# Performance work log

Measured on AMD Instinct MI355X. Metric: run time of the kernel, lower is better.

Reference implementation:

```python
import jax, jax.numpy as jnp
import numpy as np

# dims
L, E, D, DFF, H = 4, 4, 512, 2048, 8
B, T, S, K = 16, 256, 512, 2
HD = D // H


def _ln(x, g, b, eps=1e-5):
    m = x.mean(-1, keepdims=True)
    v = ((x - m) ** 2).mean(-1, keepdims=True)
    return (x - m) / jnp.sqrt(v + eps) * g + b


def _mha(xq, xkv, in_w, in_b, out_w, out_b):
    # torch nn.MultiheadAttention (batch_first), no masks, eval mode
    qw, kw, vw = jnp.split(in_w, 3, axis=0)
    qb, kb, vb = jnp.split(in_b, 3)
    q = xq @ qw.T + qb                       # [B,T,D]
    k = xkv @ kw.T + kb                      # [B,S,D]
    v = xkv @ vw.T + vb
    def heads(t):
        b, s, _ = t.shape
        return t.reshape(b, s, H, HD).transpose(0, 2, 1, 3)
    q, k, v = heads(q), heads(k), heads(v)   # [B,H,*,HD]
    scale = 1.0 / float(np.sqrt(HD))
    a = jax.nn.softmax(jnp.einsum('bhtd,bhsd->bhts', q, k) * scale, axis=-1)
    o = jnp.einsum('bhts,bhsd->bhtd', a, v)
    o = o.transpose(0, 2, 1, 3).reshape(xq.shape[0], xq.shape[1], D)
    return o @ out_w.T + out_b


def _expert(p, x, mem):
    (siw, sib, sow, sob, ciw, cib, cow, cob,
     l1w, l1b, l2w, l2b, g1, b1, g2, b2, g3, b3) = p
    sa = _mha(x, x, siw, sib, sow, sob)
    x = _ln(x + sa, g1, b1)
    ca = _mha(x, mem, ciw, cib, cow, cob)
    x = _ln(x + ca, g2, b2)
    ffn = jax.nn.relu(x @ l1w.T + l1b) @ l2w.T + l2b
    x = _ln(x + ffn, g3, b3)
    return x


def _forward(tgt, memory, router_w, params):
    x = tgt
    for l in range(L):
        pooled = x.mean(axis=1)                      # [B,D] sample-level routing
        logits = pooled @ router_w[l].T              # [B,E]
        vals, idx = jax.lax.top_k(logits, K)
        w = jax.nn.softmax(vals.astype(jnp.float32), axis=-1).astype(x.dtype)
        # dense [B,E] combine weights: zero for unselected experts -> same math
        wf = jnp.zeros((x.shape[0], E), x.dtype).at[jnp.arange(x.shape[0])[:, None], idx].add(w)
        p_l = jax.tree_util.tree_map(lambda a: a[l], params)   # each [E,...]
        outs = jax.vmap(_expert, in_axes=(0, None, None))(p_l, x, memory)  # [E,B,T,D]
        x = jnp.einsum('be,ebtd->btd', wf, outs)
    return x


def setup_inputs() -> dict:
    key = jax.random.key(0)
    ks = jax.random.split(key, 16)
    n = lambda k, shape: jax.random.normal(k, shape, jnp.float32) * 0.02
    return {
        'tgt': jax.random.normal(ks[0], (B, T, D), jnp.float32),
        'memory': jax.random.normal(ks[1], (B, S, D), jnp.float32),
        'router_w': n(ks[2], (L, E, D)),
        'sa_in_w': n(ks[3], (L, E, 3 * D, D)), 'sa_in_b': jnp.zeros((L, E, 3 * D)),
        'sa_out_w': n(ks[4], (L, E, D, D)), 'sa_out_b': jnp.zeros((L, E, D)),
        'ca_in_w': n(ks[5], (L, E, 3 * D, D)), 'ca_in_b': jnp.zeros((L, E, 3 * D)),
        'ca_out_w': n(ks[6], (L, E, D, D)), 'ca_out_b': jnp.zeros((L, E, D)),
        'lin1_w': n(ks[7], (L, E, DFF, D)), 'lin1_b': jnp.zeros((L, E, DFF)),
        'lin2_w': n(ks[8], (L, E, D, DFF)), 'lin2_b': jnp.zeros((L, E, D)),
        'n1_g': jnp.ones((L, E, D)), 'n1_b': jnp.zeros((L, E, D)),
        'n2_g': jnp.ones((L, E, D)), 'n2_b': jnp.zeros((L, E, D)),
        'n3_g': jnp.ones((L, E, D)), 'n3_b': jnp.zeros((L, E, D)),
    }


def reference(tgt, memory, router_w, sa_in_w, sa_in_b, sa_out_w, sa_out_b,
              ca_in_w, ca_in_b, ca_out_w, ca_out_b, lin1_w, lin1_b, lin2_w, lin2_b,
              n1_g, n1_b, n2_g, n2_b, n3_g, n3_b):
    params = (sa_in_w, sa_in_b, sa_out_w, sa_out_b, ca_in_w, ca_in_b, ca_out_w, ca_out_b,
              lin1_w, lin1_b, lin2_w, lin2_b, n1_g, n1_b, n2_g, n2_b, n3_g, n3_b)
    return _forward(tgt, memory, router_w, params)
```

## Files before the change

kernel.cpp:

```cpp
#include <hip/hip_runtime.h>
#include <hip/hip_bf16.h>

#define L_ 4
#define E_ 4
#define D_ 512
#define DFF_ 2048
#define H_ 8
#define B_ 16
#define T_ 256
#define S_ 512
#define HD_ 64
#define NSLOT 32

typedef __attribute__((ext_vector_type(4))) float f32x4;
typedef __attribute__((ext_vector_type(8))) short bf16x8;
typedef __attribute__((ext_vector_type(4))) int i32x4;

static __device__ __forceinline__ float bf2f(unsigned short u){
  union{float f; unsigned u;} c; c.u = ((unsigned)u)<<16; return c.f;
}
static __device__ __forceinline__ unsigned short f2bf(float f){
  union{float f; unsigned u;} c; c.f=f;
  unsigned u=c.u;
  return (unsigned short)((u + 0x7FFFu + ((u>>16)&1u))>>16);
}

static __device__ __forceinline__ void gload16(const unsigned short* g, unsigned short* l){
  __builtin_amdgcn_global_load_lds(
      (const __attribute__((address_space(1))) void*)g,
      (__attribute__((address_space(3))) void*)l, 16, 0, 0);
}

static __device__ __forceinline__ int xcd_swz(int orig, int nwg){
  int q = nwg >> 3, r = nwg & 7;
  int xcd = orig & 7, idx = orig >> 3;
  return (xcd < r) ? (xcd*(q+1) + idx) : (r*(q+1) + (xcd-r)*q + idx);
}

__global__ void __launch_bounds__(256) pool_k(const float* __restrict__ x,
    float* __restrict__ part)
{
  int b = blockIdx.x >> 3, ch = blockIdx.x & 7;
  int tid = threadIdx.x;
  const float* xp = x + ((long)b*T_ + ch*32)*D_ + tid*2;
  float s0=0.f, s1=0.f;
  #pragma unroll 8
  for (int t=0;t<32;t++){
    float2 v = *(const float2*)(xp + (long)t*D_);
    s0 += v.x; s1 += v.y;
  }
  float* pp = part + ((long)b*8 + ch)*D_ + tid*2;
  pp[0]=s0; pp[1]=s1;
}

__global__ void __launch_bounds__(256) route2_k(const float* __restrict__ part,
    const float* __restrict__ rw, int* __restrict__ eidx, float* __restrict__ wgt)
{
  __shared__ float pooled[D_];
  __shared__ float logit[E_];
  int b = blockIdx.x, tid = threadIdx.x;
  for (int d = tid; d < D_; d += 256){
    float s = 0.f;
    #pragma unroll
    for (int c=0;c<8;c++) s += part[((long)b*8 + c)*D_ + d];
    pooled[d] = s * (1.f/T_);
  }
  __syncthreads();
  int wave = tid>>6, lane = tid&63;
  {
    float s=0.f;
    const float* w = rw + (long)wave*D_;
    for (int d=lane; d<D_; d+=64) s += pooled[d]*w[d];
    #pragma unroll
    for (int o=32;o;o>>=1) s += __shfl_xor(s,o);
    if (lane==0) logit[wave] = s;
  }
  __syncthreads();
  if (tid==0){
    int i1=0; float v1=logit[0];
    for (int e=1;e<E_;e++) if (logit[e] > v1){ v1=logit[e]; i1=e; }
    int i2=-1; float v2=-3.4e38f;
    for (int e=0;e<E_;e++) if (e!=i1 && logit[e] > v2){ v2=logit[e]; i2=e; }
    float e2 = __expf(v2 - v1);
    float w1 = 1.f/(1.f+e2);
    eidx[2*b]=i1; eidx[2*b+1]=i2;
    wgt[2*b]=w1; wgt[2*b+1]=e2*w1;
  }
}

__global__ void __launch_bounds__(256) cast_bf16_k(const float* __restrict__ in,
    unsigned short* __restrict__ out, long n){
  long i = ((long)blockIdx.x*blockDim.x + threadIdx.x)*4;
  long st = (long)gridDim.x*blockDim.x*4;
  for (; i<n; i+=st){
    float4 v = *(const float4*)(in+i);
    ushort4 o; o.x=f2bf(v.x); o.y=f2bf(v.y); o.z=f2bf(v.z); o.w=f2bf(v.w);
    *(ushort4*)(out+i) = o;
  }
}

__global__ void __launch_bounds__(256) cast_weights_k(
    const float* __restrict__ s0, const float* __restrict__ s1,
    const float* __restrict__ s2, const float* __restrict__ s3,
    const float* __restrict__ s4, const float* __restrict__ s5,
    unsigned short* __restrict__ d0, unsigned short* __restrict__ d1,
    unsigned short* __restrict__ d2, unsigned short* __restrict__ d3,
    unsigned short* __restrict__ d4, unsigned short* __restrict__ d5)
{
  const long N0=(long)E_*3*D_*D_, N1=(long)E_*D_*D_;
  const long N2=N0, N3=N1, N4=(long)E_*DFF_*D_, N5=N4;
  const long total = N0+N1+N2+N3+N4+N5;
  long i = ((long)blockIdx.x*256 + threadIdx.x)*4;
  long st = (long)gridDim.x*256*4;
  for (; i<total; i+=st){
    const float* s; unsigned short* d; long j = i;
    if (j < N0){ s=s0; d=d0; }
    else if ((j-=N0) < N1){ s=s1; d=d1; }
    else if ((j-=N1) < N2){ s=s2; d=d2; }
    else if ((j-=N2) < N3){ s=s3; d=d3; }
    else if ((j-=N3) < N4){ s=s4; d=d4; }
    else { j-=N4; s=s5; d=d5; }
    float4 v = *(const float4*)(s+j);
    ushort4 o; o.x=f2bf(v.x); o.y=f2bf(v.y); o.z=f2bf(v.z); o.w=f2bf(v.w);
    *(ushort4*)(d+j) = o;
  }
}

__global__ void __launch_bounds__(256) vtrans2_k(
    const unsigned short* __restrict__ src0, long sSlot0, int ld0,
    unsigned short* __restrict__ dst0, int rows0,
    const unsigned short* __restrict__ src1, long sSlot1, int ld1,
    unsigned short* __restrict__ dst1, int rows1)
{
  __shared__ unsigned short t[64][68];
  int xb = blockIdx.x;
  const unsigned short* src; long sSlot; int ld; unsigned short* dst; int rows; int s0;
  if (xb < rows0/64){ src=src0; sSlot=sSlot0; ld=ld0; dst=dst0; rows=rows0; s0=xb*64; }
  else              { src=src1; sSlot=sSlot1; ld=ld1; dst=dst1; rows=rows1; s0=(xb-rows0/64)*64; }
  int h = blockIdx.y; int slot = blockIdx.z;
  const unsigned short* sp = src + (long)slot*sSlot + (long)h*64;
  int c = threadIdx.x&63, w = threadIdx.x>>6;
  #pragma unroll
  for (int i=0;i<16;i++){
    int r = i*4 + w;
    t[r][c] = sp[(long)(s0+r)*ld + c];
  }
  __syncthreads();
  unsigned short* dp = dst + ((long)slot*H_ + h)*((long)64*rows) + s0;
  #pragma unroll
  for (int i=0;i<16;i++){
    int d = i*4 + w;
    dp[(long)d*rows + c] = t[c][d];
  }
}

template<int NT>
__global__ void __launch_bounds__(512) fattn_k(
    const unsigned short* __restrict__ Qg, long qSlot, int ldq,
    const unsigned short* __restrict__ Kg, long kSlot, int ldk,
    const unsigned short* __restrict__ Vtg,
    unsigned short* __restrict__ Og, long oSlot, int ldo)
{
  constexpr int SLEN = NT*64;
  constexpr int NT2 = NT/2;
  __shared__ unsigned short K_lds[128][72];
  __shared__ unsigned short V_lds[64][136];
  __shared__ unsigned short P_lds[8][16][72];

  int nwg = gridDim.x*gridDim.y;
  int wg = xcd_swz(blockIdx.x + gridDim.x*blockIdx.y, nwg);
  int qb = wg % gridDim.x;
  int z  = wg / gridDim.x;
  int slot = z >> 3, h = z & 7;
  int tid = threadIdx.x, wave = tid>>6, lane = tid&63;
  int lr = lane&15, lg = lane>>4;
  int lk = lg*8;

  const unsigned short* Qp = Qg + (long)slot*qSlot + (long)h*HD_;
  const unsigned short* Kp = Kg + (long)slot*kSlot + (long)h*HD_;
  const unsigned short* Vp = Vtg + (long)z*((long)HD_*SLEN);

  bf16x8 qf[2];
  {
    int qrow = qb*128 + wave*16 + lr;
    const unsigned short* qr = Qp + (long)qrow*ldq;
    qf[0] = *(const bf16x8*)(qr + lk);
    qf[1] = *(const bf16x8*)(qr + 32 + lk);
  }

  float m_prev[4], l_run[4];
  f32x4 acc_o[4];
  #pragma unroll
  for (int r=0;r<4;r++){ m_prev[r]=-1e30f; l_run[r]=0.f; }
  #pragma unroll
  for (int ni=0;ni<4;ni++) acc_o[ni]=(f32x4){0.f,0.f,0.f,0.f};

  int srow = tid>>3, sch = tid&7;

  i32x4 kr0 = *(const i32x4*)(Kp + (long)srow*ldk + sch*8);
  i32x4 kr1 = *(const i32x4*)(Kp + (long)(srow+64)*ldk + sch*8);
  i32x4 vr0 = *(const i32x4*)(Vp + (long)srow*SLEN + sch*8);
  i32x4 vr1 = *(const i32x4*)(Vp + (long)srow*SLEN + 64 + sch*8);

  for (int it=0; it<NT2; ++it){
    __syncthreads();
    *(i32x4*)&K_lds[srow][sch*8] = kr0;
    *(i32x4*)&K_lds[srow+64][sch*8] = kr1;
    *(i32x4*)&V_lds[srow][sch*8] = vr0;
    *(i32x4*)&V_lds[srow][64 + sch*8] = vr1;
    __syncthreads();

    int itn = (it+1 < NT2) ? it+1 : it;
    int k0n = itn*128;
    kr0 = *(const i32x4*)(Kp + (long)(k0n+srow)*ldk + sch*8);
    kr1 = *(const i32x4*)(Kp + (long)(k0n+srow+64)*ldk + sch*8);
    vr0 = *(const i32x4*)(Vp + (long)srow*SLEN + k0n + sch*8);
    vr1 = *(const i32x4*)(Vp + (long)srow*SLEN + k0n + 64 + sch*8);

    #pragma unroll
    for (int sub=0; sub<2; ++sub){
      f32x4 s[4];
      #pragma unroll
      for (int ni=0;ni<4;ni++) s[ni]=(f32x4){0.f,0.f,0.f,0.f};
      __builtin_amdgcn_s_setprio(1);
      #pragma unroll
      for (int ki=0;ki<2;ki++){
        #pragma unroll
        for (int ni=0;ni<4;ni++){
          bf16x8 kf = *(const bf16x8*)&K_lds[sub*64 + ni*16+lr][ki*32+lk];
          s[ni] = __builtin_amdgcn_mfma_f32_16x16x32_bf16(qf[ki], kf, s[ni],0,0,0);
        }
      }
      __builtin_amdgcn_s_setprio(0);
      float tmax[4];
      #pragma unroll
      for (int r=0;r<4;r++){
        tmax[r] = fmaxf(fmaxf(s[0][r],s[1][r]),fmaxf(s[2][r],s[3][r]));
        #pragma unroll
        for (int msk=1; msk<16; msk<<=1) tmax[r]=fmaxf(tmax[r], __shfl_xor(tmax[r],msk));
      }
      bool inc = (tmax[0]>m_prev[0])|(tmax[1]>m_prev[1])|(tmax[2]>m_prev[2])|(tmax[3]>m_prev[3]);
      if (__any(inc)){
        #pragma unroll
        for (int r=0;r<4;r++){
          float mnew = fmaxf(m_prev[r], tmax[r]);
          float corr = __expf(m_prev[r]-mnew);
          m_prev[r] = mnew;
          l_run[r] *= corr;
          #pragma unroll
          for (int ni=0;ni<4;ni++) acc_o[ni][r] *= corr;
        }
      }
      float rs[4] = {0.f,0.f,0.f,0.f};
      #pragma unroll
      for (int ni=0;ni<4;ni++){
        #pragma unroll
        for (int r=0;r<4;r++){
          float p = __expf(s[ni][r]-m_prev[r]);
          rs[r] += p;
          P_lds[wave][lg*4+r][ni*16+lr] = f2bf(p);
        }
      }
      #pragma unroll
      for (int r=0;r<4;r++){
        #pragma unroll
        for (int msk=1; msk<16; msk<<=1) rs[r] += __shfl_xor(rs[r],msk);
        l_run[r] += rs[r];
      }
      __builtin_amdgcn_s_setprio(1);
      #pragma unroll
      for (int ki=0;ki<2;ki++){
        bf16x8 pf = *(const bf16x8*)&P_lds[wave][lr][ki*32+lk];
        #pragma unroll
        for (int ni=0;ni<4;ni++){
          bf16x8 vf = *(const bf16x8*)&V_lds[ni*16+lr][sub*64 + ki*32+lk];
          acc_o[ni] = __builtin_amdgcn_mfma_f32_16x16x32_bf16(pf, vf, acc_o[ni],0,0,0);
        }
      }
      __builtin_amdgcn_s_setprio(0);
    }
  }
  unsigned short* Op = Og + (long)slot*oSlot + (long)h*HD_;
  #pragma unroll
  for (int r=0;r<4;r++){
    float inv = 1.f/l_run[r];
    int q = qb*128 + wave*16 + lg*4 + r;
    #pragma unroll
    for (int ni=0;ni<4;ni++)
      Op[(long)q*ldo + ni*16 + lr] = f2bf(acc_o[ni][r]*inv);
  }
}

template<int BM, int BN, int WTM, int WTN, int BK>
static __device__ __forceinline__ void gemm_core(
    const unsigned short* __restrict__ Ap,
    const unsigned short* __restrict__ Wp,
    const float* __restrict__ bp,
    void* __restrict__ Cp, long cbase, int ldc,
    int lda, int ldw, int bm0, int bn0,
    int K, int f32out, int relu, int scaleNlim, float scaleVal,
    unsigned short* smem)
{
  constexpr int WAVES_N = BN/WTN;
  constexpr int MI = WTM/16, NI = WTN/16;
  constexpr int SLOTS = BK/8;
  int tid  = threadIdx.x;
  int wave = tid>>6, lane = tid&63;
  int wm = wave / WAVES_N, wn = wave % WAVES_N;
  int lr = lane&15;
  int lg = lane>>4;
  int swz = (BK==64) ? (lr&7) : ((lr>>1)&3);

  f32x4 acc[MI][NI];
  #pragma unroll
  for (int i=0;i<MI;i++)
  #pragma unroll
  for (int j=0;j<NI;j++) acc[i][j] = (f32x4){0.f,0.f,0.f,0.f};

  auto stage = [&](int buf, int k0){
    unsigned short* as = &smem[(size_t)buf*(BM+BN)*BK];
    unsigned short* bs = as + BM*BK;
    #pragma unroll
    for (int i=0;i<BM*SLOTS/512;i++){
      int cch = i*512 + tid;
      int row = cch / SLOTS, c = cch % SLOTS;
      int cs = (BK==64) ? (c ^ (row&7)) : (c ^ ((row>>1)&3));
      gload16(Ap + (long)row*lda + k0 + (cs<<3), as + cch*8);
    }
    #pragma unroll
    for (int i=0;i<BN*SLOTS/512;i++){
      int cch = i*512 + tid;
      int row = cch / SLOTS, c = cch % SLOTS;
      int cs = (BK==64) ? (c ^ (row&7)) : (c ^ ((row>>1)&3));
      gload16(Wp + (long)row*ldw + k0 + (cs<<3), bs + cch*8);
    }
  };

  auto compute = [&](int buf){
    unsigned short* as = &smem[(size_t)buf*(BM+BN)*BK];
    unsigned short* bs = as + BM*BK;
    #pragma unroll
    for (int ki=0;ki<BK/32;ki++){
      bf16x8 af[MI], bfr[NI];
      #pragma unroll
      for (int mi=0;mi<MI;mi++){
        int row = wm*WTM + mi*16 + lr;
        af[mi] = *(const bf16x8*)&as[row*BK + (((ki*4+lg) ^ swz)<<3)];
      }
      #pragma unroll
      for (int ni=0;ni<NI;ni++){
        int row = wn*WTN + ni*16 + lr;
        bfr[ni] = *(const bf16x8*)&bs[row*BK + (((ki*4+lg) ^ swz)<<3)];
      }
      __builtin_amdgcn_s_setprio(1);
      #pragma unroll
      for (int mi=0;mi<MI;mi++)
      #pragma unroll
      for (int ni=0;ni<NI;ni++)
        acc[mi][ni] = __builtin_amdgcn_mfma_f32_16x16x32_bf16(af[mi], bfr[ni], acc[mi][ni], 0,0,0);
      __builtin_amdgcn_s_setprio(0);
    }
  };

  int NT = K / BK;
  stage(0, 0);
  __syncthreads();
  int cur = 0;
  for (int t=0; t<NT; ++t){
    if (t+1 < NT) stage(cur^1, (t+1)*BK);
    compute(cur);
    __syncthreads();
    cur ^= 1;
  }

  int rbase = lg*4;
  #pragma unroll
  for (int mi=0;mi<MI;mi++)
  #pragma unroll
  for (int ni=0;ni<NI;ni++){
    f32x4 v = acc[mi][ni];
    int n = bn0 + wn*WTN + ni*16 + lr;
    float bv = bp ? bp[n] : 0.f;
    float scv = (n < scaleNlim) ? scaleVal : 1.f;
    #pragma unroll
    for (int r=0;r<4;r++){
      int m = bm0 + wm*WTM + mi*16 + rbase + r;
      float val = (v[r] + bv) * scv;
      if (relu) val = fmaxf(val, 0.f);
      long o = cbase + (long)m*ldc + n;
      if (f32out) ((float*)Cp)[o] = val;
      else ((unsigned short*)Cp)[o] = f2bf(val);
    }
  }
}

template<int BM, int BN, int WTM, int WTN, int BK>
__global__ void __launch_bounds__(512) gemm_lds(
    const unsigned short* __restrict__ A, long aSlot, int aDiv, long aHead, int lda,
    const unsigned short* __restrict__ W, long wSlot, long wHead, long wExp, int ldw,
    const int* __restrict__ eidx, const float* __restrict__ bias, long biasExp,
    void* __restrict__ Cp, long cSlot, long cHead, int ldc,
    int K, int HZ, int f32out, int relu, int scaleNlim, float scaleVal)
{
  constexpr int SLOTS = BK/8;
  static_assert((BM/WTM)*(BN/WTN) == 8, "8 waves");
  static_assert((BM*SLOTS)%512==0 && (BN*SLOTS)%512==0, "stage coverage");
  __shared__ unsigned short smem[2*(BM+BN)*BK];

  int nwg = gridDim.x*gridDim.y*gridDim.z;
  int wg = xcd_swz(blockIdx.x + gridDim.x*(blockIdx.y + gridDim.y*blockIdx.z), nwg);
  int bx = wg % gridDim.x; int t1 = wg / gridDim.x;
  int by = t1 % gridDim.y; int z  = t1 / gridDim.y;

  int slot = z / HZ;
  int h = z - slot*HZ;
  int e = eidx ? eidx[slot] : 0;
  const unsigned short* Ap = A + (long)(slot/aDiv)*aSlot + (long)h*aHead + (long)by*BM*lda;
  const unsigned short* Wp = W + (long)slot*wSlot + (long)h*wHead + (long)e*wExp + (long)bx*BN*ldw;
  const float* bp = bias ? (bias + (long)e*biasExp) : nullptr;
  long cbase = (long)slot*cSlot + (long)h*cHead;

  gemm_core<BM,BN,WTM,WTN,BK>(Ap, Wp, bp, Cp, cbase, ldc, lda, ldw,
      by*BM, bx*BN, K, f32out, relu, scaleNlim, scaleVal, smem);
}

__global__ void __launch_bounds__(512) gemm_dual(
    const unsigned short* __restrict__ A0, long aSlot0,
    const unsigned short* __restrict__ W0, const float* __restrict__ bias0,
    unsigned short* __restrict__ C0, long cSlot0, int ldc0,
    const unsigned short* __restrict__ A1, long aSlot1,
    const unsigned short* __restrict__ W1, const float* __restrict__ bias1,
    unsigned short* __restrict__ C1, long cSlot1, int ldc1,
    const int* __restrict__ eidx)
{
  constexpr int BM=128, BN=256, WTM=64, WTN=64, BK=32;
  __shared__ unsigned short smem[2*(BM+BN)*BK];
  const int NBLK0 = 6*2*NSLOT;
  int nwg = gridDim.x;
  int wg = xcd_swz(blockIdx.x, nwg);

  const unsigned short *Ap, *Wp; const float* bp;
  unsigned short* Cp; long cbase; int ldc, bm0, bn0, scaleNlim;
  if (wg < NBLK0){
    int bx = wg % 6; int t1 = wg / 6;
    int by = t1 % 2; int slot = t1 / 2;
    int e = eidx[slot];
    bm0 = by*BM; bn0 = bx*BN;
    Ap = A0 + (long)(slot/2)*aSlot0 + (long)bm0*D_;
    Wp = W0 + (long)e*(3*D_*D_) + (long)bn0*D_;
    bp = bias0 + (long)e*(3*D_);
    Cp = C0; cbase = (long)slot*cSlot0; ldc = ldc0; scaleNlim = D_;
  } else {
    int w1 = wg - NBLK0;
    int bx = w1 % 4; int t1 = w1 / 4;
    int by = t1 % 4; int slot = t1 / 4;
    int e = eidx[slot];
    bm0 = by*BM; bn0 = bx*BN;
    Ap = A1 + (long)(slot/2)*aSlot1 + (long)bm0*D_;
    Wp = W1 + (long)e*(3*D_*D_) + (long)bn0*D_;
    bp = bias1 + (long)e*(3*D_);
    Cp = C1; cbase = (long)slot*cSlot1; ldc = ldc1; scaleNlim = 0;
  }
  gemm_core<BM,BN,WTM,WTN,BK>(Ap, Wp, bp, Cp, cbase, ldc, D_, D_,
      bm0, bn0, 512, 0, 0, scaleNlim, 0.125f, smem);
}

template<int ABF>
__global__ void __launch_bounds__(256) add_ln_k(
    const void* __restrict__ Ab_, int aDiv, long aStride,
    const unsigned short* __restrict__ Bb, long bStride,
    const float* __restrict__ G, const float* __restrict__ Bt,
    const int* __restrict__ eidx,
    unsigned short* __restrict__ OutB)
{
  int row = blockIdx.x*4 + (threadIdx.x>>6);
  int slot = row>>8, t = row&255;
  int lane = threadIdx.x&63;
  int d0 = lane*8;
  float x[8];
  if (ABF){
    const unsigned short* a = (const unsigned short*)Ab_ + (long)(slot/aDiv)*aStride + (long)t*D_ + d0;
    ushort4 a0 = *(const ushort4*)a, a1 = *(const ushort4*)(a+4);
    x[0]=bf2f(a0.x); x[1]=bf2f(a0.y); x[2]=bf2f(a0.z); x[3]=bf2f(a0.w);
    x[4]=bf2f(a1.x); x[5]=bf2f(a1.y); x[6]=bf2f(a1.z); x[7]=bf2f(a1.w);
  } else {
    const float* a = (const float*)Ab_ + (long)(slot/aDiv)*aStride + (long)t*D_ + d0;
    float4 a0 = *(const float4*)a, a1 = *(const float4*)(a+4);
    x[0]=a0.x; x[1]=a0.y; x[2]=a0.z; x[3]=a0.w;
    x[4]=a1.x; x[5]=a1.y; x[6]=a1.z; x[7]=a1.w;
  }
  const unsigned short* b = Bb + (long)slot*bStride + (long)t*D_ + d0;
  ushort4 b0 = *(const ushort4*)b, b1 = *(const ushort4*)(b+4);
  x[0]+=bf2f(b0.x); x[1]+=bf2f(b0.y); x[2]+=bf2f(b0.z); x[3]+=bf2f(b0.w);
  x[4]+=bf2f(b1.x); x[5]+=bf2f(b1.y); x[6]+=bf2f(b1.z); x[7]+=bf2f(b1.w);
  float s=0.f;
  #pragma unroll
  for (int i=0;i<8;i++) s += x[i];
  #pragma unroll
  for (int o=32;o;o>>=1) s += __shfl_xor(s,o);
  float m = s*(1.f/D_);
  float q=0.f;
  #pragma unroll
  for (int i=0;i<8;i++){ float d=x[i]-m; q+=d*d; }
  #pragma unroll
  for (int o=32;o;o>>=1) q += __shfl_xor(q,o);
  float rs = rsqrtf(q*(1.f/D_)+1e-5f);
  int e = eidx[slot];
  const float* g  = G  + (long)e*D_ + d0;
  const float* bt = Bt + (long)e*D_ + d0;
  float4 g0 = *(const float4*)g, g1 = *(const float4*)(g+4);
  float4 t0 = *(const float4*)bt, t1 = *(const float4*)(bt+4);
  float gg[8] = {g0.x,g0.y,g0.z,g0.w,g1.x,g1.y,g1.z,g1.w};
  float tt[8] = {t0.x,t0.y,t0.z,t0.w,t1.x,t1.y,t1.z,t1.w};
  long ob = (long)slot*(T_*D_) + (long)t*D_ + d0;
  ushort4 o0, o1;
  float y0=(x[0]-m)*rs*gg[0]+tt[0], y1=(x[1]-m)*rs*gg[1]+tt[1];
  float y2=(x[2]-m)*rs*gg[2]+tt[2], y3=(x[3]-m)*rs*gg[3]+tt[3];
  float y4=(x[4]-m)*rs*gg[4]+tt[4], y5=(x[5]-m)*rs*gg[5]+tt[5];
  float y6=(x[6]-m)*rs*gg[6]+tt[6], y7=(x[7]-m)*rs*gg[7]+tt[7];
  o0.x=f2bf(y0); o0.y=f2bf(y1); o0.z=f2bf(y2); o0.w=f2bf(y3);
  o1.x=f2bf(y4); o1.y=f2bf(y5); o1.z=f2bf(y6); o1.w=f2bf(y7);
  *(ushort4*)(OutB+ob) = o0;
  *(ushort4*)(OutB+ob+4) = o1;
}

__global__ void __launch_bounds__(256) add_ln_comb_k(
    const unsigned short* __restrict__ x2b, const unsigned short* __restrict__ proj,
    const float* __restrict__ G, const float* __restrict__ Bt,
    const int* __restrict__ eidx, const float* __restrict__ wgt,
    float* __restrict__ dstF, unsigned short* __restrict__ dstB)
{
  int row = blockIdx.x*4 + (threadIdx.x>>6);
  int b = row>>8, t = row&255;
  int lane = threadIdx.x&63;
  int d0 = lane*8;
  float out[8];
  #pragma unroll
  for (int i=0;i<8;i++) out[i]=0.f;
  #pragma unroll
  for (int s2i=0;s2i<2;s2i++){
    int slot = 2*b + s2i;
    int e = eidx[slot];
    float w = wgt[slot];
    const unsigned short* a = x2b + (long)slot*(T_*D_) + (long)t*D_ + d0;
    const unsigned short* p = proj + (long)slot*(T_*D_) + (long)t*D_ + d0;
    ushort4 a0 = *(const ushort4*)a, a1 = *(const ushort4*)(a+4);
    ushort4 p0 = *(const ushort4*)p, p1 = *(const ushort4*)(p+4);
    float x[8];
    x[0]=bf2f(a0.x)+bf2f(p0.x); x[1]=bf2f(a0.y)+bf2f(p0.y);
    x[2]=bf2f(a0.z)+bf2f(p0.z); x[3]=bf2f(a0.w)+bf2f(p0.w);
    x[4]=bf2f(a1.x)+bf2f(p1.x); x[5]=bf2f(a1.y)+bf2f(p1.y);
    x[6]=bf2f(a1.z)+bf2f(p1.z); x[7]=bf2f(a1.w)+bf2f(p1.w);
    float s=0.f;
    #pragma unroll
    for (int i=0;i<8;i++) s += x[i];
    #pragma unroll
    for (int o=32;o;o>>=1) s += __shfl_xor(s,o);
    float m = s*(1.f/D_);
    float q=0.f;
    #pragma unroll
    for (int i=0;i<8;i++){ float d=x[i]-m; q+=d*d; }
    #pragma unroll
    for (int o=32;o;o>>=1) q += __shfl_xor(q,o);
    float rs = rsqrtf(q*(1.f/D_)+1e-5f);
    const float* g  = G  + (long)e*D_ + d0;
    const float* bt = Bt + (long)e*D_ + d0;
    float4 g0 = *(const float4*)g, g1 = *(const float4*)(g+4);
    float4 t0 = *(const float4*)bt, t1 = *(const float4*)(bt+4);
    float gg[8] = {g0.x,g0.y,g0.z,g0.w,g1.x,g1.y,g1.z,g1.w};
    float tt[8] = {t0.x,t0.y,t0.z,t0.w,t1.x,t1.y,t1.z,t1.w};
    #pragma unroll
    for (int i=0;i<8;i++) out[i] += w*((x[i]-m)*rs*gg[i]+tt[i]);
  }
  long ob = (long)row*D_ + d0;
  float4 f0 = {out[0],out[1],out[2],out[3]};
  float4 f1 = {out[4],out[5],out[6],out[7]};
  *(float4*)(dstF+ob) = f0;
  *(float4*)(dstF+ob+4) = f1;
  ushort4 o0, o1;
  o0.x=f2bf(out[0]); o0.y=f2bf(out[1]); o0.z=f2bf(out[2]); o0.w=f2bf(out[3]);
  o1.x=f2bf(out[4]); o1.y=f2bf(out[5]); o1.z=f2bf(out[6]); o1.w=f2bf(out[7]);
  *(ushort4*)(dstB+ob) = o0;
  *(ushort4*)(dstB+ob+4) = o1;
}

extern "C" void kernel_launch(void* const* d_in, const int* in_sizes, int n_in,
                              void* d_out, int out_size, void* d_ws, size_t ws_size,
                              hipStream_t stream)
{
  const float* tgt      = (const float*)d_in[0];
  const float* memory   = (const float*)d_in[1];
  const float* router_w = (const float*)d_in[2];
  const float* sa_in_w  = (const float*)d_in[3];
  const float* sa_in_b  = (const float*)d_in[4];
  const float* sa_out_w = (const float*)d_in[5];
  const float* sa_out_b = (const float*)d_in[6];
  const float* ca_in_w  = (const float*)d_in[7];
  const float* ca_in_b  = (const float*)d_in[8];
  const float* ca_out_w = (const float*)d_in[9];
  const float* ca_out_b = (const float*)d_in[10];
  const float* lin1_w   = (const float*)d_in[11];
  const float* lin1_b   = (const float*)d_in[12];
  const float* lin2_w   = (const float*)d_in[13];
  const float* lin2_b   = (const float*)d_in[14];
  const float* n1_g = (const float*)d_in[15];
  const float* n1_b = (const float*)d_in[16];
  const float* n2_g = (const float*)d_in[17];
  const float* n2_b = (const float*)d_in[18];
  const float* n3_g = (const float*)d_in[19];
  const float* n3_b = (const float*)d_in[20];

  char* ws = (char*)d_ws;
  size_t off = 0;
  auto alloc = [&](size_t bytes)->char*{
    char* p = ws + off; off += (bytes + 255) & ~(size_t)255; return p;
  };
  unsigned short* xb    = (unsigned short*)alloc(2ull*B_*T_*D_);
  unsigned short* memb  = (unsigned short*)alloc(2ull*B_*S_*D_);
  float*          x     = (float*)alloc(4ull*B_*T_*D_);
  float*          part  = (float*)alloc(4ull*B_*8*D_);
  int*            eidx  = (int*)alloc(4ull*NSLOT);
  float*          wgt   = (float*)alloc(4ull*NSLOT);
  unsigned short* wSaIn  = (unsigned short*)alloc(2ull*E_*3*D_*D_);
  unsigned short* wSaOut = (unsigned short*)alloc(2ull*E_*D_*D_);
  unsigned short* wCaIn  = (unsigned short*)alloc(2ull*E_*3*D_*D_);
  unsigned short* wCaOut = (unsigned short*)alloc(2ull*E_*D_*D_);
  unsigned short* wL1    = (unsigned short*)alloc(2ull*E_*DFF_*D_);
  unsigned short* wL2    = (unsigned short*)alloc(2ull*E_*D_*DFF_);
  unsigned short* qkv   = (unsigned short*)alloc(2ull*NSLOT*T_*3*D_);
  unsigned short* ffh   = (unsigned short*)alloc(2ull*NSLOT*T_*DFF_);
  unsigned short* attn  = (unsigned short*)alloc(2ull*NSLOT*T_*D_);
  unsigned short* proj  = (unsigned short*)alloc(2ull*NSLOT*T_*D_);
  unsigned short* x1b   = (unsigned short*)alloc(2ull*NSLOT*T_*D_);
  unsigned short* cq    = (unsigned short*)alloc(2ull*NSLOT*T_*D_);
  unsigned short* mkv   = (unsigned short*)alloc(2ull*NSLOT*S_*2*D_);
  unsigned short* x2b   = (unsigned short*)alloc(2ull*NSLOT*T_*D_);
  unsigned short* Vt2   = (unsigned short*)alloc(2ull*NSLOT*H_*HD_*S_);
  unsigned short* Vt1   = cq;

  cast_bf16_k<<<1024,256,0,stream>>>(tgt,    xb,   (long)B_*T_*D_);
  cast_bf16_k<<<1024,256,0,stream>>>(memory, memb, (long)B_*S_*D_);

  const float* xcur = tgt;
  for (int l=0; l<L_; ++l){
    pool_k<<<B_*8,256,0,stream>>>(xcur, part);
    route2_k<<<B_,256,0,stream>>>(part, router_w + (size_t)l*E_*D_, eidx, wgt);
    cast_weights_k<<<2048,256,0,stream>>>(
      sa_in_w  + (size_t)l*E_*3*D_*D_, sa_out_w + (size_t)l*E_*D_*D_,
      ca_in_w  + (size_t)l*E_*3*D_*D_, ca_out_w + (size_t)l*E_*D_*D_,
      lin1_w   + (size_t)l*E_*DFF_*D_, lin2_w   + (size_t)l*E_*D_*DFF_,
      wSaIn, wSaOut, wCaIn, wCaOut, wL1, wL2);

    gemm_dual<<<dim3(6*2*NSLOT + 4*4*NSLOT),512,0,stream>>>(
      xb,   (long)T_*D_, wSaIn,                sa_in_b + (size_t)l*E_*3*D_,
      qkv,  (long)T_*3*D_, 3*D_,
      memb, (long)S_*D_, wCaIn + (size_t)D_*D_, ca_in_b + (size_t)l*E_*3*D_ + D_,
      mkv,  (long)S_*2*D_, 2*D_,
      eidx);
    vtrans2_k<<<dim3(T_/64 + S_/64, H_, NSLOT),256,0,stream>>>(
      qkv + 2*D_, (long)T_*3*D_, 3*D_, Vt1, T_,
      mkv + D_,   (long)S_*2*D_, 2*D_, Vt2, S_);
    fattn_k<4><<<dim3(T_/128, NSLOT*H_),512,0,stream>>>(
      qkv, (long)T_*3*D_, 3*D_,
      qkv + D_, (long)T_*3*D_, 3*D_,
      Vt1, attn, (long)T_*D_, D_);
    gemm_lds<64,128,32,32,64><<<dim3(4,4,NSLOT),512,0,stream>>>(
      attn, (long)T_*D_, 1, 0, D_,
      wSaOut, 0, 0, (long)D_*D_, D_,
      eidx, sa_out_b + (size_t)l*E_*D_, D_,
      proj, (long)T_*D_, 0, D_,
      512, 1, 0, 0, 0, 1.f);
    add_ln_k<0><<<2048,256,0,stream>>>(xcur, 2, (long)T_*D_, proj, (long)T_*D_,
      n1_g + (size_t)l*E_*D_, n1_b + (size_t)l*E_*D_, eidx, x1b);
    gemm_lds<64,128,32,32,64><<<dim3(4,4,NSLOT),512,0,stream>>>(
      x1b, (long)T_*D_, 1, 0, D_,
      wCaIn, 0, 0, (long)3*D_*D_, D_,
      eidx, ca_in_b + (size_t)l*E_*3*D_, 3*D_,
      cq, (long)T_*D_, 0, D_,
      512, 1, 0, 0, D_, 0.125f);
    fattn_k<8><<<dim3(T_/128, NSLOT*H_),512,0,stream>>>(
      cq, (long)T_*D_, D_,
      mkv, (long)S_*2*D_, 2*D_,
      Vt2, attn, (long)T_*D_, D_);
    gemm_lds<64,128,32,32,64><<<dim3(4,4,NSLOT),512,0,stream>>>(
      attn, (long)T_*D_, 1, 0, D_,
      wCaOut, 0, 0, (long)D_*D_, D_,
      eidx, ca_out_b + (size_t)l*E_*D_, D_,
      proj, (long)T_*D_, 0, D_,
      512, 1, 0, 0, 0, 1.f);
    add_ln_k<1><<<2048,256,0,stream>>>(x1b, 1, (long)T_*D_, proj, (long)T_*D_,
      n2_g + (size_t)l*E_*D_, n2_b + (size_t)l*E_*D_, eidx, x2b);
    gemm_lds<128,256,64,64,32><<<dim3(8,2,NSLOT),512,0,stream>>>(
      x2b, (long)T_*D_, 1, 0, D_,
      wL1, 0, 0, (long)DFF_*D_, D_,
      eidx, lin1_b + (size_t)l*E_*DFF_, DFF_,
      ffh, (long)T_*DFF_, 0, DFF_,
      512, 1, 0, 1, 0, 1.f);
    gemm_lds<64,128,32,32,64><<<dim3(4,4,NSLOT),512,0,stream>>>(
      ffh, (long)T_*DFF_, 1, 0, DFF_,
      wL2, 0, 0, (long)D_*DFF_, DFF_,
      eidx, lin2_b + (size_t)l*E_*D_, D_,
      proj, (long)T_*D_, 0, D_,
      2048, 1, 0, 0, 0, 1.f);
    float* dstF = (l==L_-1) ? (float*)d_out : x;
    add_ln_comb_k<<<1024,256,0,stream>>>(x2b, proj,
      n3_g + (size_t)l*E_*D_, n3_b + (size_t)l*E_*D_, eidx, wgt, dstF, xb);
    xcur = x;
  }
}
```

Before: 930.5 us.

## Transpose V inside attention kernel and merge pooling into weight-cast launch

Removes the separate V-transpose kernel and its scratch buffer. The attention kernel now loads row-major V tiles straight from the QKV and memory-KV projection outputs and transposes them while writing into LDS. Separately, the pooling kernel is folded into the weight-cast kernel as extra blocks, which saves one launch per layer. The trade-off is scalar 2-byte scattered LDS stores in the attention inner loop, which may cause bank conflicts and add per-iteration cost.

```diff
diff --git a/kernel.cpp b/kernel.cpp
--- a/kernel.cpp
+++ b/kernel.cpp
@@ -37,69 +37,8 @@
   return (xcd < r) ? (xcd*(q+1) + idx) : (r*(q+1) + (xcd-r)*q + idx);
 }
 
-__global__ void __launch_bounds__(256) pool_k(const float* __restrict__ x,
-    float* __restrict__ part)
-{
-  int b = blockIdx.x >> 3, ch = blockIdx.x & 7;
-  int tid = threadIdx.x;
-  const float* xp = x + ((long)b*T_ + ch*32)*D_ + tid*2;
-  float s0=0.f, s1=0.f;
-  #pragma unroll 8
-  for (int t=0;t<32;t++){
-    float2 v = *(const float2*)(xp + (long)t*D_);
-    s0 += v.x; s1 += v.y;
-  }
-  float* pp = part + ((long)b*8 + ch)*D_ + tid*2;
-  pp[0]=s0; pp[1]=s1;
-}
-
-__global__ void __launch_bounds__(256) route2_k(const float* __restrict__ part,
-    const float* __restrict__ rw, int* __restrict__ eidx, float* __restrict__ wgt)
-{
-  __shared__ float pooled[D_];
-  __shared__ float logit[E_];
-  int b = blockIdx.x, tid = threadIdx.x;
-  for (int d = tid; d < D_; d += 256){
-    float s = 0.f;
-    #pragma unroll
-    for (int c=0;c<8;c++) s += part[((long)b*8 + c)*D_ + d];
-    pooled[d] = s * (1.f/T_);
-  }
-  __syncthreads();
-  int wave = tid>>6, lane = tid&63;
-  {
-    float s=0.f;
-    const float* w = rw + (long)wave*D_;
-    for (int d=lane; d<D_; d+=64) s += pooled[d]*w[d];
-    #pragma unroll
-    for (int o=32;o;o>>=1) s += __shfl_xor(s,o);
-    if (lane==0) logit[wave] = s;
-  }
-  __syncthreads();
-  if (tid==0){
-    int i1=0; float v1=logit[0];
-    for (int e=1;e<E_;e++) if (logit[e] > v1){ v1=logit[e]; i1=e; }
-    int i2=-1; float v2=-3.4e38f;
-    for (int e=0;e<E_;e++) if (e!=i1 && logit[e] > v2){ v2=logit[e]; i2=e; }
-    float e2 = __expf(v2 - v1);
-    float w1 = 1.f/(1.f+e2);
-    eidx[2*b]=i1; eidx[2*b+1]=i2;
-    wgt[2*b]=w1; wgt[2*b+1]=e2*w1;
-  }
-}
-
-__global__ void __launch_bounds__(256) cast_bf16_k(const float* __restrict__ in,
-    unsigned short* __restrict__ out, long n){
-  long i = ((long)blockIdx.x*blockDim.x + threadIdx.x)*4;
-  long st = (long)gridDim.x*blockDim.x*4;
-  for (; i<n; i+=st){
-    float4 v = *(const float4*)(in+i);
-    ushort4 o; o.x=f2bf(v.x); o.y=f2bf(v.y); o.z=f2bf(v.z); o.w=f2bf(v.w);
-    *(ushort4*)(out+i) = o;
-  }
-}
-
-__global__ void __launch_bounds__(256) cast_weights_k(
+__global__ void __launch_bounds__(256) prep_k(const float* __restrict__ x,
+    float* __restrict__ part,
     const float* __restrict__ s0, const float* __restrict__ s1,
     const float* __restrict__ s2, const float* __restrict__ s3,
     const float* __restrict__ s4, const float* __restrict__ s5,
@@ -107,11 +46,25 @@
     unsigned short* __restrict__ d2, unsigned short* __restrict__ d3,
     unsigned short* __restrict__ d4, unsigned short* __restrict__ d5)
 {
+  int tid = threadIdx.x;
+  if (blockIdx.x < B_*8){
+    int b = blockIdx.x >> 3, ch = blockIdx.x & 7;
+    const float* xp = x + ((long)b*T_ + ch*32)*D_ + tid*2;
+    float p0=0.f, p1=0.f;
+    #pragma unroll 8
+    for (int t=0;t<32;t++){
+      float2 v = *(const float2*)(xp + (long)t*D_);
+      p0 += v.x; p1 += v.y;
+    }
+    float* pp = part + ((long)b*8 + ch)*D_ + tid*2;
+    pp[0]=p0; pp[1]=p1;
+    return;
+  }
   const long N0=(long)E_*3*D_*D_, N1=(long)E_*D_*D_;
   const long N2=N0, N3=N1, N4=(long)E_*DFF_*D_, N5=N4;
   const long total = N0+N1+N2+N3+N4+N5;
-  long i = ((long)blockIdx.x*256 + threadIdx.x)*4;
-  long st = (long)gridDim.x*256*4;
+  long i = ((long)(blockIdx.x - B_*8)*256 + tid)*4;
+  long st = (long)(gridDim.x - B_*8)*256*4;
   for (; i<total; i+=st){
     const float* s; unsigned short* d; long j = i;
     if (j < N0){ s=s0; d=d0; }
@@ -126,31 +79,49 @@
   }
 }
 
-__global__ void __launch_bounds__(256) vtrans2_k(
-    const unsigned short* __restrict__ src0, long sSlot0, int ld0,
-    unsigned short* __restrict__ dst0, int rows0,
-    const unsigned short* __restrict__ src1, long sSlot1, int ld1,
-    unsigned short* __restrict__ dst1, int rows1)
-{
-  __shared__ unsigned short t[64][68];
-  int xb = blockIdx.x;
-  const unsigned short* src; long sSlot; int ld; unsigned short* dst; int rows; int s0;
-  if (xb < rows0/64){ src=src0; sSlot=sSlot0; ld=ld0; dst=dst0; rows=rows0; s0=xb*64; }
-  else              { src=src1; sSlot=sSlot1; ld=ld1; dst=dst1; rows=rows1; s0=(xb-rows0/64)*64; }
-  int h = blockIdx.y; int slot = blockIdx.z;
-  const unsigned short* sp = src + (long)slot*sSlot + (long)h*64;
-  int c = threadIdx.x&63, w = threadIdx.x>>6;
-  #pragma unroll
-  for (int i=0;i<16;i++){
-    int r = i*4 + w;
-    t[r][c] = sp[(long)(s0+r)*ld + c];
+__global__ void __launch_bounds__(256) route2_k(const float* __restrict__ part,
+    const float* __restrict__ rw, int* __restrict__ eidx, float* __restrict__ wgt)
+{
+  __shared__ float pooled[D_];
+  __shared__ float logit[E_];
+  int b = blockIdx.x, tid = threadIdx.x;
+  for (int d = tid; d < D_; d += 256){
+    float s = 0.f;
+    #pragma unroll
+    for (int c=0;c<8;c++) s += part[((long)b*8 + c)*D_ + d];
+    pooled[d] = s * (1.f/T_);
   }
   __syncthreads();
-  unsigned short* dp = dst + ((long)slot*H_ + h)*((long)64*rows) + s0;
-  #pragma unroll
-  for (int i=0;i<16;i++){
-    int d = i*4 + w;
-    dp[(long)d*rows + c] = t[c][d];
+  int wave = tid>>6, lane = tid&63;
+  {
+    float s=0.f;
+    const float* w = rw + (long)wave*D_;
+    for (int d=lane; d<D_; d+=64) s += pooled[d]*w[d];
+    #pragma unroll
+    for (int o=32;o;o>>=1) s += __shfl_xor(s,o);
+    if (lane==0) logit[wave] = s;
+  }
+  __syncthreads();
+  if (tid==0){
+    int i1=0; float v1=logit[0];
+    for (int e=1;e<E_;e++) if (logit[e] > v1){ v1=logit[e]; i1=e; }
+    int i2=-1; float v2=-3.4e38f;
+    for (int e=0;e<E_;e++) if (e!=i1 && logit[e] > v2){ v2=logit[e]; i2=e; }
+    float e2 = __expf(v2 - v1);
+    float w1 = 1.f/(1.f+e2);
+    eidx[2*b]=i1; eidx[2*b+1]=i2;
+    wgt[2*b]=w1; wgt[2*b+1]=e2*w1;
+  }
+}
+
+__global__ void __launch_bounds__(256) cast_bf16_k(const float* __restrict__ in,
+    unsigned short* __restrict__ out, long n){
+  long i = ((long)blockIdx.x*blockDim.x + threadIdx.x)*4;
+  long st = (long)gridDim.x*blockDim.x*4;
+  for (; i<n; i+=st){
+    float4 v = *(const float4*)(in+i);
+    ushort4 o; o.x=f2bf(v.x); o.y=f2bf(v.y); o.z=f2bf(v.z); o.w=f2bf(v.w);
+    *(ushort4*)(out+i) = o;
   }
 }
 
@@ -158,10 +129,9 @@
 __global__ void __launch_bounds__(512) fattn_k(
     const unsigned short* __restrict__ Qg, long qSlot, int ldq,
     const unsigned short* __restrict__ Kg, long kSlot, int ldk,
-    const unsigned short* __restrict__ Vtg,
+    const unsigned short* __restrict__ Vg, long vSlot, int ldv,
     unsigned short* __restrict__ Og, long oSlot, int ldo)
 {
-  constexpr int SLEN = NT*64;
   constexpr int NT2 = NT/2;
   __shared__ unsigned short K_lds[128][72];
   __shared__ unsigned short V_lds[64][136];
@@ -178,7 +148,7 @@
 
   const unsigned short* Qp = Qg + (long)slot*qSlot + (long)h*HD_;
   const unsigned short* Kp = Kg + (long)slot*kSlot + (long)h*HD_;
-  const unsigned short* Vp = Vtg + (long)z*((long)HD_*SLEN);
+  const unsigned short* Vp = Vg + (long)slot*vSlot + (long)h*HD_;
 
   bf16x8 qf[2];
   {
@@ -199,23 +169,30 @@
 
   i32x4 kr0 = *(const i32x4*)(Kp + (long)srow*ldk + sch*8);
   i32x4 kr1 = *(const i32x4*)(Kp + (long)(srow+64)*ldk + sch*8);
-  i32x4 vr0 = *(const i32x4*)(Vp + (long)srow*SLEN + sch*8);
-  i32x4 vr1 = *(const i32x4*)(Vp + (long)srow*SLEN + 64 + sch*8);
+  i32x4 vr0 = *(const i32x4*)(Vp + (long)srow*ldv + sch*8);
+  i32x4 vr1 = *(const i32x4*)(Vp + (long)(srow+64)*ldv + sch*8);
 
   for (int it=0; it<NT2; ++it){
     __syncthreads();
     *(i32x4*)&K_lds[srow][sch*8] = kr0;
     *(i32x4*)&K_lds[srow+64][sch*8] = kr1;
-    *(i32x4*)&V_lds[srow][sch*8] = vr0;
-    *(i32x4*)&V_lds[srow][64 + sch*8] = vr1;
+    {
+      const unsigned short* p0 = (const unsigned short*)&vr0;
+      const unsigned short* p1 = (const unsigned short*)&vr1;
+      #pragma unroll
+      for (int j=0;j<8;j++){
+        V_lds[sch*8+j][srow]      = p0[j];
+        V_lds[sch*8+j][srow+64]   = p1[j];
+      }
+    }
     __syncthreads();
 
     int itn = (it+1 < NT2) ? it+1 : it;
     int k0n = itn*128;
     kr0 = *(const i32x4*)(Kp + (long)(k0n+srow)*ldk + sch*8);
     kr1 = *(const i32x4*)(Kp + (long)(k0n+srow+64)*ldk + sch*8);
-    vr0 = *(const i32x4*)(Vp + (long)srow*SLEN + k0n + sch*8);
-    vr1 = *(const i32x4*)(Vp + (long)srow*SLEN + k0n + 64 + sch*8);
+    vr0 = *(const i32x4*)(Vp + (long)(k0n+srow)*ldv + sch*8);
+    vr1 = *(const i32x4*)(Vp + (long)(k0n+srow+64)*ldv + sch*8);
 
     #pragma unroll
     for (int sub=0; sub<2; ++sub){
@@ -635,21 +612,18 @@
   unsigned short* cq    = (unsigned short*)alloc(2ull*NSLOT*T_*D_);
   unsigned short* mkv   = (unsigned short*)alloc(2ull*NSLOT*S_*2*D_);
   unsigned short* x2b   = (unsigned short*)alloc(2ull*NSLOT*T_*D_);
-  unsigned short* Vt2   = (unsigned short*)alloc(2ull*NSLOT*H_*HD_*S_);
-  unsigned short* Vt1   = cq;
 
   cast_bf16_k<<<1024,256,0,stream>>>(tgt,    xb,   (long)B_*T_*D_);
   cast_bf16_k<<<1024,256,0,stream>>>(memory, memb, (long)B_*S_*D_);
 
   const float* xcur = tgt;
   for (int l=0; l<L_; ++l){
-    pool_k<<<B_*8,256,0,stream>>>(xcur, part);
-    route2_k<<<B_,256,0,stream>>>(part, router_w + (size_t)l*E_*D_, eidx, wgt);
-    cast_weights_k<<<2048,256,0,stream>>>(
+    prep_k<<<B_*8 + 2048,256,0,stream>>>(xcur, part,
       sa_in_w  + (size_t)l*E_*3*D_*D_, sa_out_w + (size_t)l*E_*D_*D_,
       ca_in_w  + (size_t)l*E_*3*D_*D_, ca_out_w + (size_t)l*E_*D_*D_,
       lin1_w   + (size_t)l*E_*DFF_*D_, lin2_w   + (size_t)l*E_*D_*DFF_,
       wSaIn, wSaOut, wCaIn, wCaOut, wL1, wL2);
+    route2_k<<<B_,256,0,stream>>>(part, router_w + (size_t)l*E_*D_, eidx, wgt);
 
     gemm_dual<<<dim3(6*2*NSLOT + 4*4*NSLOT),512,0,stream>>>(
       xb,   (long)T_*D_, wSaIn,                sa_in_b + (size_t)l*E_*3*D_,
@@ -657,13 +631,11 @@
       memb, (long)S_*D_, wCaIn + (size_t)D_*D_, ca_in_b + (size_t)l*E_*3*D_ + D_,
       mkv,  (long)S_*2*D_, 2*D_,
       eidx);
-    vtrans2_k<<<dim3(T_/64 + S_/64, H_, NSLOT),256,0,stream>>>(
-      qkv + 2*D_, (long)T_*3*D_, 3*D_, Vt1, T_,
-      mkv + D_,   (long)S_*2*D_, 2*D_, Vt2, S_);
     fattn_k<4><<<dim3(T_/128, NSLOT*H_),512,0,stream>>>(
       qkv, (long)T_*3*D_, 3*D_,
       qkv + D_, (long)T_*3*D_, 3*D_,
-      Vt1, attn, (long)T_*D_, D_);
+      qkv + 2*D_, (long)T_*3*D_, 3*D_,
+      attn, (long)T_*D_, D_);
     gemm_lds<64,128,32,32,64><<<dim3(4,4,NSLOT),512,0,stream>>>(
       attn, (long)T_*D_, 1, 0, D_,
       wSaOut, 0, 0, (long)D_*D_, D_,
@@ -681,7 +653,8 @@
     fattn_k<8><<<dim3(T_/128, NSLOT*H_),512,0,stream>>>(
       cq, (long)T_*D_, D_,
       mkv, (long)S_*2*D_, 2*D_,
-      Vt2, attn, (long)T_*D_, D_);
+      mkv + D_, (long)S_*2*D_, 2*D_,
+      attn, (long)T_*D_, D_);
     gemm_lds<64,128,32,32,64><<<dim3(4,4,NSLOT),512,0,stream>>>(
       attn, (long)T_*D_, 1, 0, D_,
       wCaOut, 0, 0, (long)D_*D_, D_,
```

Result: no change. 930.1 us (-0.0%).
